# Kernel optimization log

Measured on AMD Instinct MI355X. Metric: run time of the kernel, lower is better.

Reference implementation:

```python
import jax, jax.numpy as jnp
import numpy as np

ALPHA = 0.5  # config_param['alpha']


def setup_inputs() -> dict:
    key = jax.random.key(0)
    ks = jax.random.split(key, 10)
    B, T, N, E, H = 64, 20, 8192, 128, 128
    # sparse multi-hot basket indicators
    x = (jax.random.uniform(ks[0], (B, T, N)) < 0.01).astype(jnp.float32)
    seq_len = jax.random.randint(ks[1], (B,), 1, T + 1)  # pack_padded requires >=1
    A = jax.random.uniform(ks[2], (N, N), dtype=jnp.float32) * 0.01  # dense item-item adjacency
    W1 = jax.random.normal(ks[3], (E, N), dtype=jnp.float32) * 0.02
    b1 = jnp.zeros((E,), jnp.float32)
    W2 = jax.random.normal(ks[4], (E, N), dtype=jnp.float32) * 0.02
    b2 = jnp.zeros((E,), jnp.float32)
    W_ih = jax.random.normal(ks[5], (4 * H, E), dtype=jnp.float32) * 0.05
    W_hh = jax.random.normal(ks[6], (4 * H, H), dtype=jnp.float32) * 0.05
    b_ih = jnp.zeros((4 * H,), jnp.float32)
    b_hh = jnp.zeros((4 * H,), jnp.float32)
    W_out = jax.random.normal(ks[7], (N, H), dtype=jnp.float32) * 0.02
    I_B = jnp.ones((N,), jnp.float32) / N  # item_probs-style bias init
    threshold = jnp.array([0.005], jnp.float32)  # adj_matrix.mean()
    return dict(x=x, seq_len=seq_len, A=A, W1=W1, b1=b1, W2=W2, b2=b2,
                W_ih=W_ih, W_hh=W_hh, b_ih=b_ih, b_hh=b_hh,
                W_out=W_out, I_B=I_B, threshold=threshold)


def reference(x, seq_len, A, W1, b1, W2, b2, W_ih, W_hh, b_ih, b_hh, W_out, I_B, threshold):
    B, T, N = x.shape
    H = W_hh.shape[1]
    xf = x.reshape(B * T, N)
    # two basket encoders, elementwise max combine (dropout = identity in eval)
    e1 = jax.nn.relu(xf @ W1.T + b1)
    e2 = jax.nn.relu(xf @ W2.T + b2)
    basket = jnp.maximum(e1, e2).reshape(B, T, -1)  # [B, T, E]

    # 1-layer LSTM (torch gate order i,f,g,o); packed variable-length seqs
    # emulated by freezing (h, c) once t >= seq_len, so h_n matches pack_padded.
    valid = jnp.arange(T)[:, None] < seq_len[None, :]  # [T, B]
    xs = basket.transpose(1, 0, 2)                     # [T, B, E]
    b = b_ih + b_hh

    def step(carry, inp):
        h, c = carry
        x_t, v = inp
        gates = x_t @ W_ih.T + h @ W_hh.T + b
        i, f, g, o = jnp.split(gates, 4, axis=-1)
        c_new = jax.nn.sigmoid(f) * c + jax.nn.sigmoid(i) * jnp.tanh(g)
        h_new = jax.nn.sigmoid(o) * jnp.tanh(c_new)
        m = v[:, None]
        return (jnp.where(m, h_new, h), jnp.where(m, c_new, c)), None

    h0 = jnp.zeros((B, H), x.dtype)
    c0 = jnp.zeros((B, H), x.dtype)
    (h_n, _), _ = jax.lax.scan(step, (h0, c0), (xs, valid))

    p = jax.nn.sigmoid(h_n @ W_out.T)  # [B, N]
    # mm(p, diag(relu(I_B))) is algebraically an elementwise scale
    predict = (1.0 - ALPHA) * p + ALPHA * (p * jax.nn.relu(I_B) + jax.nn.relu(p @ A))
    return predict
```

## Files before the change

kernel.cpp:

```cpp
#include <hip/hip_runtime.h>
#include <hip/hip_bf16.h>
#include <stdint.h>

#define B_ 64
#define T_ 20
#define N_ 8192
#define E_ 128
#define H_ 128
#define G4 512

typedef short bf16x8 __attribute__((ext_vector_type(8)));
typedef float f32x4 __attribute__((ext_vector_type(4)));

__device__ __forceinline__ float sigmoidf_(float x){ return 1.0f/(1.0f+expf(-x)); }

__device__ __forceinline__ unsigned short f2bf(float f){
  union { float f; uint32_t u; } v; v.f = f;
  uint32_t u = v.u;
  uint32_t r = (u + 0x7FFFu + ((u >> 16) & 1u)) >> 16;
  return (unsigned short)r;
}
__device__ __forceinline__ uint32_t pk2(float a, float b){
  return (uint32_t)f2bf(a) | ((uint32_t)f2bf(b) << 16);
}

__global__ void k_transpose(const float* __restrict__ W1, const float* __restrict__ W2,
                            float* __restrict__ W12T){
  __shared__ float t1[128][33];
  __shared__ float t2[128][33];
  int n0 = blockIdx.x * 32;
  int tid = threadIdx.x;
  int nl = tid & 31, eg = tid >> 5;
  for (int i = 0; i < 16; i++){
    int e = eg * 16 + i;
    t1[e][nl] = W1[(size_t)e*N_ + n0 + nl];
    t2[e][nl] = W2[(size_t)e*N_ + n0 + nl];
  }
  __syncthreads();
  for (int n = 0; n < 32; n++){
    float v = (tid < 128) ? t1[tid][n] : t2[tid-128][n];
    W12T[(size_t)(n0+n)*256 + tid] = v;
  }
}

__global__ void k_mlp(const float* __restrict__ x, const int* __restrict__ seq_len,
                      const float* __restrict__ W12T, const float* __restrict__ b1,
                      const float* __restrict__ b2, float* __restrict__ basket){
  int bt = blockIdx.x;
  int b = bt / T_, t = bt % T_;
  if (t >= seq_len[b]) return;
  __shared__ int idxs[1024];
  __shared__ int cnt;
  __shared__ float e2s[128];
  int tid = threadIdx.x;
  if (tid == 0) cnt = 0;
  __syncthreads();
  const float4* xr = (const float4*)(x + (size_t)bt * N_);
  for (int i = 0; i < 8; i++){
    float4 v = xr[i*256 + tid];
    int base = (i*256 + tid)*4;
    if (v.x != 0.f){ int q = atomicAdd(&cnt,1); idxs[q] = base;   }
    if (v.y != 0.f){ int q = atomicAdd(&cnt,1); idxs[q] = base+1; }
    if (v.z != 0.f){ int q = atomicAdd(&cnt,1); idxs[q] = base+2; }
    if (v.w != 0.f){ int q = atomicAdd(&cnt,1); idxs[q] = base+3; }
  }
  __syncthreads();
  int m = cnt; if (m > 1024) m = 1024;
  float acc = (tid < 128) ? b1[tid] : b2[tid-128];
  for (int i = 0; i < m; i++)
    acc += W12T[(size_t)idxs[i]*256 + tid];
  acc = fmaxf(acc, 0.f);
  if (tid >= 128) e2s[tid-128] = acc;
  __syncthreads();
  if (tid < 128) basket[(size_t)bt*E_ + tid] = fmaxf(acc, e2s[tid]);
}

__global__ void k_xproj(const int* __restrict__ seq_len, const float* __restrict__ basket,
                        const float* __restrict__ W_ih, const float* __restrict__ b_ih,
                        const float* __restrict__ b_hh, float* __restrict__ Xp){
  int bt = blockIdx.x;
  int b = bt / T_, t = bt % T_;
  if (t >= seq_len[b]) return;
  __shared__ float xv[128];
  int tid = threadIdx.x;
  if (tid < 128) xv[tid] = basket[(size_t)bt*E_ + tid];
  __syncthreads();
  const float4* wr = (const float4*)(W_ih + (size_t)tid * E_);
  float acc = b_ih[tid] + b_hh[tid];
  #pragma unroll
  for (int k4 = 0; k4 < 32; k4++){
    float4 w = wr[k4];
    float4 h = *(const float4*)&xv[k4*4];
    acc += w.x*h.x + w.y*h.y + w.z*h.z + w.w*h.w;
  }
  Xp[(size_t)bt*G4 + tid] = acc;
}

__global__ void __launch_bounds__(512, 2)
k_lstm(const int* __restrict__ seq_len, const float* __restrict__ Xp,
       const float* __restrict__ W_hh, float* __restrict__ hn){
  int b = blockIdx.x;
  int L = seq_len[b];
  int j = threadIdx.x;
  float4 whh[32];
  const float4* wr = (const float4*)(W_hh + (size_t)j * H_);
  #pragma unroll
  for (int k = 0; k < 32; k++) whh[k] = wr[k];
  __shared__ float hs[128];
  __shared__ float gs[512];
  if (j < 128) hs[j] = 0.f;
  float c = 0.f;
  __syncthreads();
  for (int t = 0; t < L; t++){
    float g = Xp[((size_t)b*T_ + t)*G4 + j];
    #pragma unroll
    for (int k = 0; k < 32; k++){
      float4 h = *(const float4*)&hs[k*4];
      float4 w = whh[k];
      g += w.x*h.x + w.y*h.y + w.z*h.z + w.w*h.w;
    }
    gs[j] = g;
    __syncthreads();
    if (j < 128){
      float i_ = gs[j], f_ = gs[128+j], gg = gs[256+j], o_ = gs[384+j];
      c = sigmoidf_(f_)*c + sigmoidf_(i_)*tanhf(gg);
      hs[j] = sigmoidf_(o_)*tanhf(c);
    }
    __syncthreads();
  }
  if (j < 128) hn[(size_t)b*H_ + j] = hs[j];
}

__global__ void k_pout(const float* __restrict__ hn, const float* __restrict__ W_out,
                       float* __restrict__ p, unsigned short* __restrict__ pbf){
  __shared__ unsigned short hb[64*128];
  int tid = threadIdx.x;
  {
    int row = tid >> 2;
    int k16 = (tid & 3) * 32;
    const float4* hr = (const float4*)(hn + (size_t)row*H_ + k16);
    #pragma unroll
    for (int i = 0; i < 4; i++){
      float4 a = hr[i*2], bq = hr[i*2+1];
      uint4 u; u.x = pk2(a.x,a.y); u.y = pk2(a.z,a.w); u.z = pk2(bq.x,bq.y); u.w = pk2(bq.z,bq.w);
      int blk = (k16 >> 3) + i;
      *(uint4*)&hb[row*128 + ((blk ^ (row & 7)) * 8)] = u;
    }
  }
  __syncthreads();
  int w = tid >> 6, l = tid & 63;
  int n0 = blockIdx.x * 128;
  f32x4 acc[8];
  #pragma unroll
  for (int i = 0; i < 8; i++) acc[i] = (f32x4){0.f,0.f,0.f,0.f};
  int row = w*16 + (l & 15);
  #pragma unroll
  for (int ks = 0; ks < 4; ks++){
    int kk = ks*32 + (l >> 4)*8;
    int blk = kk >> 3;
    bf16x8 af = *(bf16x8*)&hb[row*128 + ((blk ^ (row & 7)) * 8)];
    #pragma unroll
    for (int nt = 0; nt < 8; nt++){
      int n = n0 + nt*16 + (l & 15);
      const float4* wp = (const float4*)(W_out + (size_t)n*H_ + kk);
      float4 wa = wp[0], wb = wp[1];
      union { uint4 u; bf16x8 v; } cc;
      cc.u.x = pk2(wa.x,wa.y); cc.u.y = pk2(wa.z,wa.w);
      cc.u.z = pk2(wb.x,wb.y); cc.u.w = pk2(wb.z,wb.w);
      acc[nt] = __builtin_amdgcn_mfma_f32_16x16x32_bf16(af, cc.v, acc[nt], 0, 0, 0);
    }
  }
  #pragma unroll
  for (int nt = 0; nt < 8; nt++){
    int n = n0 + nt*16 + (l & 15);
    #pragma unroll
    for (int r = 0; r < 4; r++){
      int rr = w*16 + (l >> 4)*4 + r;
      float pv = 1.f/(1.f + expf(-acc[nt][r]));
      p[(size_t)rr*N_ + n] = pv;
      pbf[(size_t)rr*N_ + n] = f2bf(pv);
    }
  }
}

__global__ void __launch_bounds__(256, 2)
k_gemm(const unsigned short* __restrict__ pbf, const float* __restrict__ Ag,
       float* __restrict__ C){
  __shared__ unsigned short Abf[128*32];
  __shared__ unsigned short pt[64*32];
  int tid = threadIdx.x;
  int nb = blockIdx.x & 63, ks = blockIdx.x >> 6;
  int n0 = nb * 128;
  int kbase = ks * 1024;
  int w = tid >> 6, l = tid & 63;
  f32x4 acc[8];
  #pragma unroll
  for (int i = 0; i < 8; i++) acc[i] = (f32x4){0.f,0.f,0.f,0.f};
  int sn = tid & 127, kq = tid >> 7;
  int prow = tid >> 2, phw = (tid & 3) * 8;

  for (int step = 0; step < 32; step++){
    int kb = kbase + step*32;
    *(uint4*)&pt[prow*32 + phw] = *(const uint4*)&pbf[(size_t)prow*N_ + kb + phw];
    #pragma unroll
    for (int i = 0; i < 4; i++){
      int k4 = kq*16 + i*4;
      float v0 = Ag[(size_t)(kb + k4 + 0)*N_ + n0 + sn];
      float v1 = Ag[(size_t)(kb + k4 + 1)*N_ + n0 + sn];
      float v2 = Ag[(size_t)(kb + k4 + 2)*N_ + n0 + sn];
      float v3 = Ag[(size_t)(kb + k4 + 3)*N_ + n0 + sn];
      uint2 u; u.x = pk2(v0,v1); u.y = pk2(v2,v3);
      *(uint2*)&Abf[sn*32 + (k4 ^ ((sn & 3) * 8))] = u;
    }
    __syncthreads();
    bf16x8 af = *(bf16x8*)&pt[(w*16 + (l & 15))*32 + (l >> 4)*8];
    #pragma unroll
    for (int nt = 0; nt < 8; nt++){
      int n = nt*16 + (l & 15);
      bf16x8 bfr = *(bf16x8*)&Abf[n*32 + (((l >> 4)*8) ^ ((n & 3)*8))];
      acc[nt] = __builtin_amdgcn_mfma_f32_16x16x32_bf16(af, bfr, acc[nt], 0, 0, 0);
    }
    __syncthreads();
  }
  #pragma unroll
  for (int nt = 0; nt < 8; nt++){
    int n = n0 + nt*16 + (l & 15);
    #pragma unroll
    for (int r = 0; r < 4; r++){
      int rr = w*16 + (l >> 4)*4 + r;
      atomicAdd(&C[(size_t)rr*N_ + n], acc[nt][r]);
    }
  }
}

__global__ void k_final(const float* __restrict__ p, const float* __restrict__ C,
                        const float* __restrict__ I_B, float* __restrict__ out){
  int idx = blockIdx.x*256 + threadIdx.x;
  float4 pv = ((const float4*)p)[idx];
  float4 cv = ((const float4*)C)[idx];
  int n = (idx*4) & (N_-1);
  float4 ib = *(const float4*)&I_B[n];
  float4 o;
  o.x = 0.5f*pv.x + 0.5f*(pv.x*fmaxf(ib.x,0.f) + fmaxf(cv.x,0.f));
  o.y = 0.5f*pv.y + 0.5f*(pv.y*fmaxf(ib.y,0.f) + fmaxf(cv.y,0.f));
  o.z = 0.5f*pv.z + 0.5f*(pv.z*fmaxf(ib.z,0.f) + fmaxf(cv.z,0.f));
  o.w = 0.5f*pv.w + 0.5f*(pv.w*fmaxf(ib.w,0.f) + fmaxf(cv.w,0.f));
  ((float4*)out)[idx] = o;
}

extern "C" void kernel_launch(void* const* d_in, const int* in_sizes, int n_in,
                              void* d_out, int out_size, void* d_ws, size_t ws_size,
                              hipStream_t stream) {
  const float* x     = (const float*)d_in[0];
  const int*   seq   = (const int*)  d_in[1];
  const float* A     = (const float*)d_in[2];
  const float* W1    = (const float*)d_in[3];
  const float* b1    = (const float*)d_in[4];
  const float* W2    = (const float*)d_in[5];
  const float* b2    = (const float*)d_in[6];
  const float* W_ih  = (const float*)d_in[7];
  const float* W_hh  = (const float*)d_in[8];
  const float* b_ih  = (const float*)d_in[9];
  const float* b_hh  = (const float*)d_in[10];
  const float* W_out = (const float*)d_in[11];
  const float* I_B   = (const float*)d_in[12];
  float* out = (float*)d_out;

  float* ws     = (float*)d_ws;
  float* W12T   = ws;
  float* basket = W12T + 2097152;
  float* Xp     = basket + 163840;
  float* hn     = Xp + 655360;
  float* p      = hn + 8192;
  float* C      = p + 524288;
  unsigned short* pbf = (unsigned short*)(C + 524288);

  hipMemsetAsync(C, 0, 524288*sizeof(float), stream);
  k_transpose<<<256, 256, 0, stream>>>(W1, W2, W12T);
  k_mlp      <<<1280,256, 0, stream>>>(x, seq, W12T, b1, b2, basket);
  k_xproj    <<<1280,512, 0, stream>>>(seq, basket, W_ih, b_ih, b_hh, Xp);
  k_lstm     <<<64,  512, 0, stream>>>(seq, Xp, W_hh, hn);
  k_pout     <<<64,  256, 0, stream>>>(hn, W_out, p, pbf);
  k_gemm     <<<512, 256, 0, stream>>>(pbf, A, C);
  k_final    <<<512, 256, 0, stream>>>(p, C, I_B, out);
}
```

Baseline: 169.4 us.

## Fuse basket MLP with input projection, raise GEMM split-K, drop fp32 p buffer

```diff
diff --git a/kernel.cpp b/kernel.cpp
--- a/kernel.cpp
+++ b/kernel.cpp
@@ -8,6 +8,7 @@
 #define E_ 128
 #define H_ 128
 #define G4 512
+#define SPLITK 16
 
 typedef short bf16x8 __attribute__((ext_vector_type(8)));
 typedef float f32x4 __attribute__((ext_vector_type(4)));
@@ -23,6 +24,9 @@
 __device__ __forceinline__ uint32_t pk2(float a, float b){
   return (uint32_t)f2bf(a) | ((uint32_t)f2bf(b) << 16);
 }
+__device__ __forceinline__ float bf2f(unsigned short s){
+  union { uint32_t u; float f; } v; v.u = ((uint32_t)s) << 16; return v.f;
+}
 
 __global__ void k_transpose(const float* __restrict__ W1, const float* __restrict__ W2,
                             float* __restrict__ W12T){
@@ -43,15 +47,18 @@
   }
 }
 
-__global__ void k_mlp(const float* __restrict__ x, const int* __restrict__ seq_len,
-                      const float* __restrict__ W12T, const float* __restrict__ b1,
-                      const float* __restrict__ b2, float* __restrict__ basket){
+__global__ void k_mlpx(const float* __restrict__ x, const int* __restrict__ seq_len,
+                       const float* __restrict__ W12T, const float* __restrict__ b1,
+                       const float* __restrict__ b2, const float* __restrict__ W_ih,
+                       const float* __restrict__ b_ih, const float* __restrict__ b_hh,
+                       float* __restrict__ Xp){
   int bt = blockIdx.x;
   int b = bt / T_, t = bt % T_;
   if (t >= seq_len[b]) return;
   __shared__ int idxs[1024];
   __shared__ int cnt;
   __shared__ float e2s[128];
+  __shared__ float bx[128];
   int tid = threadIdx.x;
   if (tid == 0) cnt = 0;
   __syncthreads();
@@ -72,28 +79,23 @@
   acc = fmaxf(acc, 0.f);
   if (tid >= 128) e2s[tid-128] = acc;
   __syncthreads();
-  if (tid < 128) basket[(size_t)bt*E_ + tid] = fmaxf(acc, e2s[tid]);
-}
-
-__global__ void k_xproj(const int* __restrict__ seq_len, const float* __restrict__ basket,
-                        const float* __restrict__ W_ih, const float* __restrict__ b_ih,
-                        const float* __restrict__ b_hh, float* __restrict__ Xp){
-  int bt = blockIdx.x;
-  int b = bt / T_, t = bt % T_;
-  if (t >= seq_len[b]) return;
-  __shared__ float xv[128];
-  int tid = threadIdx.x;
-  if (tid < 128) xv[tid] = basket[(size_t)bt*E_ + tid];
-  __syncthreads();
-  const float4* wr = (const float4*)(W_ih + (size_t)tid * E_);
-  float acc = b_ih[tid] + b_hh[tid];
-  #pragma unroll
-  for (int k4 = 0; k4 < 32; k4++){
-    float4 w = wr[k4];
-    float4 h = *(const float4*)&xv[k4*4];
-    acc += w.x*h.x + w.y*h.y + w.z*h.z + w.w*h.w;
-  }
-  Xp[(size_t)bt*G4 + tid] = acc;
+  if (tid < 128) bx[tid] = fmaxf(acc, e2s[tid]);
+  __syncthreads();
+  #pragma unroll
+  for (int half = 0; half < 2; half++){
+    int j = half*256 + tid;
+    const float4* wr = (const float4*)(W_ih + (size_t)j * E_);
+    float s0 = b_ih[j] + b_hh[j], s1 = 0.f, s2 = 0.f, s3 = 0.f;
+    #pragma unroll
+    for (int k4 = 0; k4 < 32; k4 += 4){
+      float4 w, h;
+      w = wr[k4+0]; h = *(const float4*)&bx[k4*4+ 0]; s0 += w.x*h.x + w.y*h.y + w.z*h.z + w.w*h.w;
+      w = wr[k4+1]; h = *(const float4*)&bx[k4*4+ 4]; s1 += w.x*h.x + w.y*h.y + w.z*h.z + w.w*h.w;
+      w = wr[k4+2]; h = *(const float4*)&bx[k4*4+ 8]; s2 += w.x*h.x + w.y*h.y + w.z*h.z + w.w*h.w;
+      w = wr[k4+3]; h = *(const float4*)&bx[k4*4+12]; s3 += w.x*h.x + w.y*h.y + w.z*h.z + w.w*h.w;
+    }
+    Xp[(size_t)bt*G4 + j] = (s0 + s1) + (s2 + s3);
+  }
 }
 
 __global__ void __launch_bounds__(512, 2)
@@ -112,14 +114,16 @@
   float c = 0.f;
   __syncthreads();
   for (int t = 0; t < L; t++){
-    float g = Xp[((size_t)b*T_ + t)*G4 + j];
-    #pragma unroll
-    for (int k = 0; k < 32; k++){
-      float4 h = *(const float4*)&hs[k*4];
-      float4 w = whh[k];
-      g += w.x*h.x + w.y*h.y + w.z*h.z + w.w*h.w;
-    }
-    gs[j] = g;
+    float s0 = Xp[((size_t)b*T_ + t)*G4 + j], s1 = 0.f, s2 = 0.f, s3 = 0.f;
+    #pragma unroll
+    for (int k = 0; k < 32; k += 4){
+      float4 w, h;
+      w = whh[k+0]; h = *(const float4*)&hs[k*4+ 0]; s0 += w.x*h.x + w.y*h.y + w.z*h.z + w.w*h.w;
+      w = whh[k+1]; h = *(const float4*)&hs[k*4+ 4]; s1 += w.x*h.x + w.y*h.y + w.z*h.z + w.w*h.w;
+      w = whh[k+2]; h = *(const float4*)&hs[k*4+ 8]; s2 += w.x*h.x + w.y*h.y + w.z*h.z + w.w*h.w;
+      w = whh[k+3]; h = *(const float4*)&hs[k*4+12]; s3 += w.x*h.x + w.y*h.y + w.z*h.z + w.w*h.w;
+    }
+    gs[j] = (s0 + s1) + (s2 + s3);
     __syncthreads();
     if (j < 128){
       float i_ = gs[j], f_ = gs[128+j], gg = gs[256+j], o_ = gs[384+j];
@@ -132,7 +136,7 @@
 }
 
 __global__ void k_pout(const float* __restrict__ hn, const float* __restrict__ W_out,
-                       float* __restrict__ p, unsigned short* __restrict__ pbf){
+                       unsigned short* __restrict__ pbf){
   __shared__ unsigned short hb[64*128];
   int tid = threadIdx.x;
   {
@@ -177,13 +181,12 @@
     for (int r = 0; r < 4; r++){
       int rr = w*16 + (l >> 4)*4 + r;
       float pv = 1.f/(1.f + expf(-acc[nt][r]));
-      p[(size_t)rr*N_ + n] = pv;
       pbf[(size_t)rr*N_ + n] = f2bf(pv);
     }
   }
 }
 
-__global__ void __launch_bounds__(256, 2)
+__global__ void __launch_bounds__(256, 4)
 k_gemm(const unsigned short* __restrict__ pbf, const float* __restrict__ Ag,
        float* __restrict__ C){
   __shared__ unsigned short Abf[128*32];
@@ -191,7 +194,7 @@
   int tid = threadIdx.x;
   int nb = blockIdx.x & 63, ks = blockIdx.x >> 6;
   int n0 = nb * 128;
-  int kbase = ks * 1024;
+  int kbase = ks * (N_ / SPLITK);
   int w = tid >> 6, l = tid & 63;
   f32x4 acc[8];
   #pragma unroll
@@ -199,7 +202,7 @@
   int sn = tid & 127, kq = tid >> 7;
   int prow = tid >> 2, phw = (tid & 3) * 8;
 
-  for (int step = 0; step < 32; step++){
+  for (int step = 0; step < (N_ / SPLITK) / 32; step++){
     int kb = kbase + step*32;
     *(uint4*)&pt[prow*32 + phw] = *(const uint4*)&pbf[(size_t)prow*N_ + kb + phw];
     #pragma unroll
@@ -233,18 +236,19 @@
   }
 }
 
-__global__ void k_final(const float* __restrict__ p, const float* __restrict__ C,
+__global__ void k_final(const unsigned short* __restrict__ pbf, const float* __restrict__ C,
                         const float* __restrict__ I_B, float* __restrict__ out){
   int idx = blockIdx.x*256 + threadIdx.x;
-  float4 pv = ((const float4*)p)[idx];
+  ushort4 pu = ((const ushort4*)pbf)[idx];
   float4 cv = ((const float4*)C)[idx];
   int n = (idx*4) & (N_-1);
   float4 ib = *(const float4*)&I_B[n];
   float4 o;
-  o.x = 0.5f*pv.x + 0.5f*(pv.x*fmaxf(ib.x,0.f) + fmaxf(cv.x,0.f));
-  o.y = 0.5f*pv.y + 0.5f*(pv.y*fmaxf(ib.y,0.f) + fmaxf(cv.y,0.f));
-  o.z = 0.5f*pv.z + 0.5f*(pv.z*fmaxf(ib.z,0.f) + fmaxf(cv.z,0.f));
-  o.w = 0.5f*pv.w + 0.5f*(pv.w*fmaxf(ib.w,0.f) + fmaxf(cv.w,0.f));
+  float p0 = bf2f(pu.x), p1 = bf2f(pu.y), p2 = bf2f(pu.z), p3 = bf2f(pu.w);
+  o.x = 0.5f*p0 + 0.5f*(p0*fmaxf(ib.x,0.f) + fmaxf(cv.x,0.f));
+  o.y = 0.5f*p1 + 0.5f*(p1*fmaxf(ib.y,0.f) + fmaxf(cv.y,0.f));
+  o.z = 0.5f*p2 + 0.5f*(p2*fmaxf(ib.z,0.f) + fmaxf(cv.z,0.f));
+  o.w = 0.5f*p3 + 0.5f*(p3*fmaxf(ib.w,0.f) + fmaxf(cv.w,0.f));
   ((float4*)out)[idx] = o;
 }
 
@@ -268,19 +272,16 @@
 
   float* ws     = (float*)d_ws;
   float* W12T   = ws;
-  float* basket = W12T + 2097152;
-  float* Xp     = basket + 163840;
+  float* Xp     = W12T + 2097152;
   float* hn     = Xp + 655360;
-  float* p      = hn + 8192;
-  float* C      = p + 524288;
+  float* C      = hn + 8192;
   unsigned short* pbf = (unsigned short*)(C + 524288);
 
   hipMemsetAsync(C, 0, 524288*sizeof(float), stream);
   k_transpose<<<256, 256, 0, stream>>>(W1, W2, W12T);
-  k_mlp      <<<1280,256, 0, stream>>>(x, seq, W12T, b1, b2, basket);
-  k_xproj    <<<1280,512, 0, stream>>>(seq, basket, W_ih, b_ih, b_hh, Xp);
+  k_mlpx     <<<1280,256, 0, stream>>>(x, seq, W12T, b1, b2, W_ih, b_ih, b_hh, Xp);
   k_lstm     <<<64,  512, 0, stream>>>(seq, Xp, W_hh, hn);
-  k_pout     <<<64,  256, 0, stream>>>(hn, W_out, p, pbf);
-  k_gemm     <<<512, 256, 0, stream>>>(pbf, A, C);
-  k_final    <<<512, 256, 0, stream>>>(p, C, I_B, out);
-}
+  k_pout     <<<64,  256, 0, stream>>>(hn, W_out, pbf);
+  k_gemm     <<<64*SPLITK, 256, 0, stream>>>(pbf, A, C);
+  k_final    <<<512, 256, 0, stream>>>(pbf, C, I_B, out);
+}
```

Result: slower. 192.6 us (+13.7%).
